# Kernel tuning notes

Hardware: AMD Instinct MI355X
Metric: run time of the kernel (lower is better)

## Reference

```python
import jax, jax.numpy as jnp
import numpy as np

B, K, C, H, W = 4, 100, 8, 128, 128
P = (C + 2) * C + C + C * C + C + C + 1  # 169 dynamic params per instance


def setup_inputs() -> dict:
    key = jax.random.key(0)
    k1, k2, k3 = jax.random.split(key, 3)
    seg_feat = jax.random.normal(k1, (B, C, H, W), dtype=jnp.float32)
    conv_weight = jax.random.normal(k2, (B, P, H, W), dtype=jnp.float32) * 0.1
    ind = jax.random.randint(k3, (B, K), 0, H * W)
    return {"seg_feat": seg_feat, "conv_weight": conv_weight, "ind": ind}


def _mask_head(seg_feat, conv_weight, ind):
    Bq, Cc, Hh, Ww = seg_feat.shape
    Kk = ind.shape[1]
    n = Bq * Kk
    HWl = Hh * Ww

    # _tranpose_and_gather_feat: [B,P,H,W] -> [B,HW,P] -> gather at ind -> [n,P]
    cw = conv_weight.reshape(Bq, -1, HWl).transpose(0, 2, 1)  # B,HW,P
    params = jnp.take_along_axis(cw, ind[:, :, None], axis=1).reshape(n, -1)

    # instance locations (x = ind % W, y = ind // W)
    xi = (ind % Ww).astype(jnp.float32)
    yi = (ind // Ww).astype(jnp.float32)
    loc = jnp.stack([xi, yi], axis=-1).reshape(n, 2)  # n,2

    # coords map, row-major (y outer, x inner), columns (x, y)
    y_grid, x_grid = jnp.meshgrid(jnp.arange(Hh, dtype=jnp.float32),
                                  jnp.arange(Ww, dtype=jnp.float32), indexing="ij")
    coords = jnp.stack([x_grid.reshape(-1), y_grid.reshape(-1)], axis=1)  # HW,2

    rel = (loc[:, None, :] - coords[None, :, :]).transpose(0, 2, 1) / 128.0  # n,2,HW

    # per-instance features: mask_feats[im_inds] -> [n, C, HW]
    feats = jnp.broadcast_to(seg_feat.reshape(Bq, 1, Cc, HWl), (Bq, Kk, Cc, HWl)).reshape(n, Cc, HWl)

    x = jnp.concatenate([rel, feats], axis=1)  # n, C+2, HW

    # parse dynamic params: weight_nums=[(C+2)*C, C*C, C], bias_nums=[C, C, 1]
    s0 = (Cc + 2) * Cc
    s1 = s0 + Cc * Cc
    s2 = s1 + Cc
    w0 = params[:, :s0].reshape(n, Cc, Cc + 2)
    w1 = params[:, s0:s1].reshape(n, Cc, Cc)
    w2 = params[:, s1:s2].reshape(n, 1, Cc)
    b0 = params[:, s2:s2 + Cc]
    b1 = params[:, s2 + Cc:s2 + 2 * Cc]
    b2 = params[:, s2 + 2 * Cc:]

    # grouped 1x1 convs == per-instance batched GEMMs
    h = jax.nn.relu(jnp.einsum("noc,ncL->noL", w0, x) + b0[:, :, None])
    h = jax.nn.relu(jnp.einsum("noc,ncL->noL", w1, h) + b1[:, :, None])
    logits = jnp.einsum("noc,ncL->noL", w2, h) + b2[:, :, None]  # n,1,HW
    return logits.reshape(Bq, Kk, Hh, Ww)


def reference(seg_feat, conv_weight, ind):
    logits = _mask_head(seg_feat, conv_weight, ind)
    return jax.nn.sigmoid(logits)  # B, K, H, W (is_train=False path)
```

## Files before the change

kernel.cpp:

```cpp
#include <hip/hip_runtime.h>
#include <hip/hip_fp16.h>
#include <math.h>

typedef unsigned int u32;
typedef __attribute__((ext_vector_type(8))) _Float16 f16x8;
typedef __attribute__((ext_vector_type(16))) float f32x16;

#define HW 16384
#define NB 4
#define NK 100
#define NGRP 25

__device__ __forceinline__ u32 pk2h(float lo, float hi) {
    return (u32)__half_as_ushort(__float2half_rn(lo))
         | ((u32)__half_as_ushort(__float2half_rn(hi)) << 16);
}
__device__ __forceinline__ void swap32(u32 &a, u32 &b) {
    asm("v_permlane32_swap_b32 %0, %1" : "+v"(a), "+v"(b));
}
__device__ __forceinline__ float rcpf(float x) {
    float r; asm("v_rcp_f32 %0, %1" : "=v"(r) : "v"(x)); return r;
}

__global__ __launch_bounds__(256) void pack_kernel(
    const float* __restrict__ cw, const int* __restrict__ ind,
    u32* __restrict__ A0, u32* __restrict__ A1, float* __restrict__ WT)
{
    int id = blockIdx.x * 256 + threadIdx.x;
    if (id < 25600) {
        int bg = id >> 8, rem = id & 255;
        int lane = rem >> 2, reg = rem & 3;
        int b = bg / NGRP, g = bg % NGRP;
        int row = lane & 31;
        int inst = g * 4 + (row >> 3);
        int ch = row & 7;
        int hw = ind[b * NK + inst];
        const float* base = cw + (size_t)b * 169 * HW + hw;
        float sx = (float)(hw & 127), sy = (float)(hw >> 7);
        float v[2];
        #pragma unroll
        for (int j = 0; j < 2; ++j) {
            int k = ((lane >> 5) << 3) + reg * 2 + j;
            float val = 0.f;
            if (k < 2)
                val = -base[(size_t)(ch * 10 + k) * HW] * 0.0078125f;
            else if (k < 10)
                val = base[(size_t)(ch * 10 + k) * HW];
            else if (k == 10)
                val = base[(size_t)(152 + ch) * HW]
                    + (base[(size_t)(ch * 10) * HW] * sx
                     + base[(size_t)(ch * 10 + 1) * HW] * sy) * 0.0078125f;
            v[j] = val;
        }
        A0[id] = pk2h(v[0], v[1]);
    } else if (id < 76800) {
        int id2 = id - 25600;
        int bg = id2 >> 9, r2 = id2 & 511;
        int frag = r2 >> 8;
        int lane = (r2 >> 2) & 63, reg = r2 & 3;
        int b = bg / NGRP, g = bg % NGRP;
        int row = lane & 31;
        int inst = g * 4 + (row >> 3);
        int hw = ind[b * NK + inst];
        const float* base = cw + (size_t)b * 169 * HW + hw;
        float v[2];
        #pragma unroll
        for (int j = 0; j < 2; ++j) {
            int k = ((lane >> 5) << 3) + reg * 2 + j;
            bool valid = ((row >> 4) == frag) && (((row >> 3) & 1) == (k >> 3));
            v[j] = valid ? base[(size_t)(80 + (row & 7) * 8 + (k & 7)) * HW] : 0.f;
        }
        A1[id2] = pk2h(v[0], v[1]);
    } else if (id < 84800) {
        int id3 = id - 76800;
        int bg = id3 / 80, q = id3 - bg * 80;
        int b = bg / NGRP, g = bg % NGRP;
        float val = 0.f;
        if (q < 32) {
            int hi = q >> 4, e = q & 15;
            int row = (e & 3) + 8 * (e >> 2) + 4 * hi;
            int inst = g * 4 + (row >> 3);
            int hw = ind[b * NK + inst];
            val = cw[(size_t)b * 169 * HW + (size_t)(160 + (row & 7)) * HW + hw];
        } else if (q < 64) {
            int half = (q - 32) >> 4, q2 = (q - 32) & 15;
            int n = q2 >> 2, j = q2 & 3;
            int hw = ind[b * NK + g * 4 + n];
            val = cw[(size_t)b * 169 * HW + (size_t)(144 + half * 4 + j) * HW + hw];
        } else if (q < 68) {
            int n = q - 64;
            int hw = ind[b * NK + g * 4 + n];
            val = 0.5f * cw[(size_t)b * 169 * HW + (size_t)168 * HW + hw];
        }
        WT[id3] = val;
    }
}

__global__ __launch_bounds__(64, 4) void mfma_kernel(
    const float* __restrict__ seg_feat,
    const u32* __restrict__ A0, const u32* __restrict__ A1,
    const float* __restrict__ WT, float* __restrict__ out)
{
    const int lane = threadIdx.x;
    const bool hi = lane >= 32;
    const int col = lane & 31;
    const int tile = blockIdx.x;
    const int b = blockIdx.y;
    const int g0 = blockIdx.z * 13;
    const int g1 = blockIdx.z ? NGRP : 13;

    const int px = tile * 32 + col;

    float f[8];
    #pragma unroll
    for (int c = 0; c < 8; ++c)
        f[c] = seg_feat[(size_t)(b * 8 + c) * HW + px];
    const float xp = (float)(px & 127), yp = (float)(px >> 7);

    u32 b0w0 = hi ? pk2h(f[6], f[7]) : pk2h(xp, yp);
    u32 b0w1 = hi ? 0x00003C00u : pk2h(f[0], f[1]);
    u32 b0w2 = hi ? 0u : pk2h(f[2], f[3]);
    u32 b0w3 = hi ? 0u : pk2h(f[4], f[5]);
    uint4 b0u = make_uint4(b0w0, b0w1, b0w2, b0w3);
    f16x8 B0 = __builtin_bit_cast(f16x8, b0u);

    f32x16 zero;
    #pragma unroll
    for (int i = 0; i < 16; ++i) zero[i] = 0.f;

    for (int g = g0; g < g1; ++g) {
        const int bg = b * NGRP + g;
        uint4 a0w  = ((const uint4*)A0)[bg * 64 + lane];
        uint4 a1aw = ((const uint4*)A1)[(bg * 2 + 0) * 64 + lane];
        uint4 a1bw = ((const uint4*)A1)[(bg * 2 + 1) * 64 + lane];
        const float* wb = WT + bg * 80;
        const float4* bi = (const float4*)(wb + (hi ? 16 : 0));
        float4 i0 = bi[0], i1 = bi[1], i2 = bi[2], i3 = bi[3];
        const float4* wv = (const float4*)(wb + 32 + (hi ? 16 : 0));
        float4 wn0 = wv[0], wn1 = wv[1], wn2 = wv[2], wn3 = wv[3];

        f32x16 d0 = __builtin_amdgcn_mfma_f32_32x32x16_f16(
            __builtin_bit_cast(f16x8, a0w), B0, zero, 0, 0, 0);

        u32 u0 = pk2h(fmaxf(d0[0], 0.f),  fmaxf(d0[1], 0.f));
        u32 u1 = pk2h(fmaxf(d0[2], 0.f),  fmaxf(d0[3], 0.f));
        u32 u2 = pk2h(fmaxf(d0[4], 0.f),  fmaxf(d0[5], 0.f));
        u32 u3 = pk2h(fmaxf(d0[6], 0.f),  fmaxf(d0[7], 0.f));
        u32 u4 = pk2h(fmaxf(d0[8], 0.f),  fmaxf(d0[9], 0.f));
        u32 u5 = pk2h(fmaxf(d0[10], 0.f), fmaxf(d0[11], 0.f));
        u32 u6 = pk2h(fmaxf(d0[12], 0.f), fmaxf(d0[13], 0.f));
        u32 u7 = pk2h(fmaxf(d0[14], 0.f), fmaxf(d0[15], 0.f));
        swap32(u0, u2);
        swap32(u1, u3);
        swap32(u4, u6);
        swap32(u5, u7);
        uint4 b1au = make_uint4(u0, u1, u2, u3);
        uint4 b1bu = make_uint4(u4, u5, u6, u7);

        f32x16 d1;
        d1[0] = i0.x; d1[1] = i0.y; d1[2]  = i0.z; d1[3]  = i0.w;
        d1[4] = i1.x; d1[5] = i1.y; d1[6]  = i1.z; d1[7]  = i1.w;
        d1[8] = i2.x; d1[9] = i2.y; d1[10] = i2.z; d1[11] = i2.w;
        d1[12] = i3.x; d1[13] = i3.y; d1[14] = i3.z; d1[15] = i3.w;
        d1 = __builtin_amdgcn_mfma_f32_32x32x16_f16(
            __builtin_bit_cast(f16x8, a1aw), __builtin_bit_cast(f16x8, b1au), d1, 0, 0, 0);
        d1 = __builtin_amdgcn_mfma_f32_32x32x16_f16(
            __builtin_bit_cast(f16x8, a1bw), __builtin_bit_cast(f16x8, b1bu), d1, 0, 0, 0);

        const float b2h0 = wb[64], b2h1 = wb[65], b2h2 = wb[66], b2h3 = wb[67];

        float pz0 = b2h0, pz1 = b2h1, pz2 = b2h2, pz3 = b2h3;
        pz0 = fmaf(wn0.x, fmaxf(d1[0], 0.f), pz0);
        pz0 = fmaf(wn0.y, fmaxf(d1[1], 0.f), pz0);
        pz0 = fmaf(wn0.z, fmaxf(d1[2], 0.f), pz0);
        pz0 = fmaf(wn0.w, fmaxf(d1[3], 0.f), pz0);
        pz1 = fmaf(wn1.x, fmaxf(d1[4], 0.f), pz1);
        pz1 = fmaf(wn1.y, fmaxf(d1[5], 0.f), pz1);
        pz1 = fmaf(wn1.z, fmaxf(d1[6], 0.f), pz1);
        pz1 = fmaf(wn1.w, fmaxf(d1[7], 0.f), pz1);
        pz2 = fmaf(wn2.x, fmaxf(d1[8], 0.f), pz2);
        pz2 = fmaf(wn2.y, fmaxf(d1[9], 0.f), pz2);
        pz2 = fmaf(wn2.z, fmaxf(d1[10], 0.f), pz2);
        pz2 = fmaf(wn2.w, fmaxf(d1[11], 0.f), pz2);
        pz3 = fmaf(wn3.x, fmaxf(d1[12], 0.f), pz3);
        pz3 = fmaf(wn3.y, fmaxf(d1[13], 0.f), pz3);
        pz3 = fmaf(wn3.z, fmaxf(d1[14], 0.f), pz3);
        pz3 = fmaf(wn3.w, fmaxf(d1[15], 0.f), pz3);

        u32 a01 = __builtin_bit_cast(u32, pz0), b01 = __builtin_bit_cast(u32, pz1);
        swap32(a01, b01);
        float z01 = __builtin_bit_cast(float, a01) + __builtin_bit_cast(float, b01);
        u32 a23 = __builtin_bit_cast(u32, pz2), b23 = __builtin_bit_cast(u32, pz3);
        swap32(a23, b23);
        float z23 = __builtin_bit_cast(float, a23) + __builtin_bit_cast(float, b23);

        float o01 = rcpf(1.f + __expf(-z01));
        float o23 = rcpf(1.f + __expf(-z23));

        size_t obase = (size_t)(b * NK + g * 4) * HW + px;
        out[obase + (size_t)(hi ? 1 : 0) * HW] = o01;
        out[obase + (size_t)(hi ? 3 : 2) * HW] = o23;
    }
}

extern "C" void kernel_launch(void* const* d_in, const int* in_sizes, int n_in,
                              void* d_out, int out_size, void* d_ws, size_t ws_size,
                              hipStream_t stream) {
    const float* seg_feat    = (const float*)d_in[0];
    const float* conv_weight = (const float*)d_in[1];
    const int*   ind         = (const int*)d_in[2];
    float*       out         = (float*)d_out;

    u32*   A0 = (u32*)d_ws;
    u32*   A1 = (u32*)((char*)d_ws + 102400);
    float* WT = (float*)((char*)d_ws + 307200);

    {
        dim3 grid((84800 + 255) / 256), block(256);
        pack_kernel<<<grid, block, 0, stream>>>(conv_weight, ind, A0, A1, WT);
    }
    {
        dim3 grid(512, 4, 2), block(64);
        mfma_kernel<<<grid, block, 0, stream>>>(seg_feat, A0, A1, WT, out);
    }
}
```

Measured before the change: 31.09 us.

## Process two pixel tiles per wave and split instance groups four ways

Each wave now handles 64 pixels, two 32-pixel MFMA tiles that share one load of the per-group packed weights and biases. This halves the weight-fetch traffic per pixel. The instance-group range is split across four z-blocks (7/6/6/6 groups) instead of two. v_permlane32_swap is replaced by __shfl_xor-based cross-half exchanges plus selects, which may cost more instructions or use LDS-backed permutes. The two independent MFMA chains per iteration also give the scheduler more instruction-level parallelism, at the price of more registers.

Result: faster. 28.52 us (-8.2%).

```diff
diff --git a/kernel.cpp b/kernel.cpp
--- a/kernel.cpp
+++ b/kernel.cpp
@@ -15,8 +15,11 @@
     return (u32)__half_as_ushort(__float2half_rn(lo))
          | ((u32)__half_as_ushort(__float2half_rn(hi)) << 16);
 }
-__device__ __forceinline__ void swap32(u32 &a, u32 &b) {
-    asm("v_permlane32_swap_b32 %0, %1" : "+v"(a), "+v"(b));
+__device__ __forceinline__ u32 sx32(u32 v) {
+    return (u32)__shfl_xor((int)v, 32, 64);
+}
+__device__ __forceinline__ float sx32f(float v) {
+    return __shfl_xor(v, 32, 64);
 }
 __device__ __forceinline__ float rcpf(float x) {
     float r; asm("v_rcp_f32 %0, %1" : "=v"(r) : "v"(x)); return r;
@@ -106,23 +109,32 @@
     const int col = lane & 31;
     const int tile = blockIdx.x;
     const int b = blockIdx.y;
-    const int g0 = blockIdx.z * 13;
-    const int g1 = blockIdx.z ? NGRP : 13;
-
-    const int px = tile * 32 + col;
-
-    float f[8];
+    const int z = blockIdx.z;
+    const int g0 = (z == 0) ? 0 : (6 * z + 1);
+    const int g1 = 6 * z + 7;
+
+    const int pxa = tile * 64 + col;
+    const int pxb = pxa + 32;
+
+    float fa[8], fb[8];
     #pragma unroll
-    for (int c = 0; c < 8; ++c)
-        f[c] = seg_feat[(size_t)(b * 8 + c) * HW + px];
-    const float xp = (float)(px & 127), yp = (float)(px >> 7);
-
-    u32 b0w0 = hi ? pk2h(f[6], f[7]) : pk2h(xp, yp);
-    u32 b0w1 = hi ? 0x00003C00u : pk2h(f[0], f[1]);
-    u32 b0w2 = hi ? 0u : pk2h(f[2], f[3]);
-    u32 b0w3 = hi ? 0u : pk2h(f[4], f[5]);
-    uint4 b0u = make_uint4(b0w0, b0w1, b0w2, b0w3);
-    f16x8 B0 = __builtin_bit_cast(f16x8, b0u);
+    for (int c = 0; c < 8; ++c) {
+        fa[c] = seg_feat[(size_t)(b * 8 + c) * HW + pxa];
+        fb[c] = seg_feat[(size_t)(b * 8 + c) * HW + pxb];
+    }
+    const float xpa = (float)(pxa & 127), ypa = (float)(pxa >> 7);
+    const float xpb = (float)(pxb & 127), ypb = (float)(pxb >> 7);
+
+    uint4 b0ua = make_uint4(hi ? pk2h(fa[6], fa[7]) : pk2h(xpa, ypa),
+                            hi ? 0x00003C00u : pk2h(fa[0], fa[1]),
+                            hi ? 0u : pk2h(fa[2], fa[3]),
+                            hi ? 0u : pk2h(fa[4], fa[5]));
+    uint4 b0ub = make_uint4(hi ? pk2h(fb[6], fb[7]) : pk2h(xpb, ypb),
+                            hi ? 0x00003C00u : pk2h(fb[0], fb[1]),
+                            hi ? 0u : pk2h(fb[2], fb[3]),
+                            hi ? 0u : pk2h(fb[4], fb[5]));
+    f16x8 B0a = __builtin_bit_cast(f16x8, b0ua);
+    f16x8 B0b = __builtin_bit_cast(f16x8, b0ub);
 
     f32x16 zero;
     #pragma unroll
@@ -138,68 +150,130 @@
         float4 i0 = bi[0], i1 = bi[1], i2 = bi[2], i3 = bi[3];
         const float4* wv = (const float4*)(wb + 32 + (hi ? 16 : 0));
         float4 wn0 = wv[0], wn1 = wv[1], wn2 = wv[2], wn3 = wv[3];
-
-        f32x16 d0 = __builtin_amdgcn_mfma_f32_32x32x16_f16(
-            __builtin_bit_cast(f16x8, a0w), B0, zero, 0, 0, 0);
-
-        u32 u0 = pk2h(fmaxf(d0[0], 0.f),  fmaxf(d0[1], 0.f));
-        u32 u1 = pk2h(fmaxf(d0[2], 0.f),  fmaxf(d0[3], 0.f));
-        u32 u2 = pk2h(fmaxf(d0[4], 0.f),  fmaxf(d0[5], 0.f));
-        u32 u3 = pk2h(fmaxf(d0[6], 0.f),  fmaxf(d0[7], 0.f));
-        u32 u4 = pk2h(fmaxf(d0[8], 0.f),  fmaxf(d0[9], 0.f));
-        u32 u5 = pk2h(fmaxf(d0[10], 0.f), fmaxf(d0[11], 0.f));
-        u32 u6 = pk2h(fmaxf(d0[12], 0.f), fmaxf(d0[13], 0.f));
-        u32 u7 = pk2h(fmaxf(d0[14], 0.f), fmaxf(d0[15], 0.f));
-        swap32(u0, u2);
-        swap32(u1, u3);
-        swap32(u4, u6);
-        swap32(u5, u7);
-        uint4 b1au = make_uint4(u0, u1, u2, u3);
-        uint4 b1bu = make_uint4(u4, u5, u6, u7);
-
-        f32x16 d1;
-        d1[0] = i0.x; d1[1] = i0.y; d1[2]  = i0.z; d1[3]  = i0.w;
-        d1[4] = i1.x; d1[5] = i1.y; d1[6]  = i1.z; d1[7]  = i1.w;
-        d1[8] = i2.x; d1[9] = i2.y; d1[10] = i2.z; d1[11] = i2.w;
-        d1[12] = i3.x; d1[13] = i3.y; d1[14] = i3.z; d1[15] = i3.w;
-        d1 = __builtin_amdgcn_mfma_f32_32x32x16_f16(
-            __builtin_bit_cast(f16x8, a1aw), __builtin_bit_cast(f16x8, b1au), d1, 0, 0, 0);
-        d1 = __builtin_amdgcn_mfma_f32_32x32x16_f16(
-            __builtin_bit_cast(f16x8, a1bw), __builtin_bit_cast(f16x8, b1bu), d1, 0, 0, 0);
-
-        const float b2h0 = wb[64], b2h1 = wb[65], b2h2 = wb[66], b2h3 = wb[67];
-
-        float pz0 = b2h0, pz1 = b2h1, pz2 = b2h2, pz3 = b2h3;
-        pz0 = fmaf(wn0.x, fmaxf(d1[0], 0.f), pz0);
-        pz0 = fmaf(wn0.y, fmaxf(d1[1], 0.f), pz0);
-        pz0 = fmaf(wn0.z, fmaxf(d1[2], 0.f), pz0);
-        pz0 = fmaf(wn0.w, fmaxf(d1[3], 0.f), pz0);
-        pz1 = fmaf(wn1.x, fmaxf(d1[4], 0.f), pz1);
-        pz1 = fmaf(wn1.y, fmaxf(d1[5], 0.f), pz1);
-        pz1 = fmaf(wn1.z, fmaxf(d1[6], 0.f), pz1);
-        pz1 = fmaf(wn1.w, fmaxf(d1[7], 0.f), pz1);
-        pz2 = fmaf(wn2.x, fmaxf(d1[8], 0.f), pz2);
-        pz2 = fmaf(wn2.y, fmaxf(d1[9], 0.f), pz2);
-        pz2 = fmaf(wn2.z, fmaxf(d1[10], 0.f), pz2);
-        pz2 = fmaf(wn2.w, fmaxf(d1[11], 0.f), pz2);
-        pz3 = fmaf(wn3.x, fmaxf(d1[12], 0.f), pz3);
-        pz3 = fmaf(wn3.y, fmaxf(d1[13], 0.f), pz3);
-        pz3 = fmaf(wn3.z, fmaxf(d1[14], 0.f), pz3);
-        pz3 = fmaf(wn3.w, fmaxf(d1[15], 0.f), pz3);
-
-        u32 a01 = __builtin_bit_cast(u32, pz0), b01 = __builtin_bit_cast(u32, pz1);
-        swap32(a01, b01);
-        float z01 = __builtin_bit_cast(float, a01) + __builtin_bit_cast(float, b01);
-        u32 a23 = __builtin_bit_cast(u32, pz2), b23 = __builtin_bit_cast(u32, pz3);
-        swap32(a23, b23);
-        float z23 = __builtin_bit_cast(float, a23) + __builtin_bit_cast(float, b23);
-
-        float o01 = rcpf(1.f + __expf(-z01));
-        float o23 = rcpf(1.f + __expf(-z23));
-
-        size_t obase = (size_t)(b * NK + g * 4) * HW + px;
-        out[obase + (size_t)(hi ? 1 : 0) * HW] = o01;
-        out[obase + (size_t)(hi ? 3 : 2) * HW] = o23;
+        float4 bw = *(const float4*)(wb + 64);
+
+        {
+            f32x16 d0 = __builtin_amdgcn_mfma_f32_32x32x16_f16(
+                __builtin_bit_cast(f16x8, a0w), B0a, zero, 0, 0, 0);
+
+            u32 u0 = pk2h(fmaxf(d0[0], 0.f),  fmaxf(d0[1], 0.f));
+            u32 u1 = pk2h(fmaxf(d0[2], 0.f),  fmaxf(d0[3], 0.f));
+            u32 u2 = pk2h(fmaxf(d0[4], 0.f),  fmaxf(d0[5], 0.f));
+            u32 u3 = pk2h(fmaxf(d0[6], 0.f),  fmaxf(d0[7], 0.f));
+            u32 u4 = pk2h(fmaxf(d0[8], 0.f),  fmaxf(d0[9], 0.f));
+            u32 u5 = pk2h(fmaxf(d0[10], 0.f), fmaxf(d0[11], 0.f));
+            u32 u6 = pk2h(fmaxf(d0[12], 0.f), fmaxf(d0[13], 0.f));
+            u32 u7 = pk2h(fmaxf(d0[14], 0.f), fmaxf(d0[15], 0.f));
+            u32 t0 = sx32(u0), t1 = sx32(u1), t2 = sx32(u2), t3 = sx32(u3);
+            u32 t4 = sx32(u4), t5 = sx32(u5), t6 = sx32(u6), t7 = sx32(u7);
+            uint4 b1au = make_uint4(hi ? t2 : u0, hi ? t3 : u1,
+                                    hi ? u2 : t0, hi ? u3 : t1);
+            uint4 b1bu = make_uint4(hi ? t6 : u4, hi ? t7 : u5,
+                                    hi ? u6 : t4, hi ? u7 : t5);
+
+            f32x16 d1;
+            d1[0]  = i0.x; d1[1]  = i0.y; d1[2]  = i0.z; d1[3]  = i0.w;
+            d1[4]  = i1.x; d1[5]  = i1.y; d1[6]  = i1.z; d1[7]  = i1.w;
+            d1[8]  = i2.x; d1[9]  = i2.y; d1[10] = i2.z; d1[11] = i2.w;
+            d1[12] = i3.x; d1[13] = i3.y; d1[14] = i3.z; d1[15] = i3.w;
+            d1 = __builtin_amdgcn_mfma_f32_32x32x16_f16(
+                __builtin_bit_cast(f16x8, a1aw), __builtin_bit_cast(f16x8, b1au), d1, 0, 0, 0);
+            d1 = __builtin_amdgcn_mfma_f32_32x32x16_f16(
+                __builtin_bit_cast(f16x8, a1bw), __builtin_bit_cast(f16x8, b1bu), d1, 0, 0, 0);
+
+            float pz0 = bw.x, pz1 = bw.y, pz2 = bw.z, pz3 = bw.w;
+            pz0 = fmaf(wn0.x, fmaxf(d1[0], 0.f), pz0);
+            pz0 = fmaf(wn0.y, fmaxf(d1[1], 0.f), pz0);
+            pz0 = fmaf(wn0.z, fmaxf(d1[2], 0.f), pz0);
+            pz0 = fmaf(wn0.w, fmaxf(d1[3], 0.f), pz0);
+            pz1 = fmaf(wn1.x, fmaxf(d1[4], 0.f), pz1);
+            pz1 = fmaf(wn1.y, fmaxf(d1[5], 0.f), pz1);
+            pz1 = fmaf(wn1.z, fmaxf(d1[6], 0.f), pz1);
+            pz1 = fmaf(wn1.w, fmaxf(d1[7], 0.f), pz1);
+            pz2 = fmaf(wn2.x, fmaxf(d1[8], 0.f), pz2);
+            pz2 = fmaf(wn2.y, fmaxf(d1[9], 0.f), pz2);
+            pz2 = fmaf(wn2.z, fmaxf(d1[10], 0.f), pz2);
+            pz2 = fmaf(wn2.w, fmaxf(d1[11], 0.f), pz2);
+            pz3 = fmaf(wn3.x, fmaxf(d1[12], 0.f), pz3);
+            pz3 = fmaf(wn3.y, fmaxf(d1[13], 0.f), pz3);
+            pz3 = fmaf(wn3.z, fmaxf(d1[14], 0.f), pz3);
+            pz3 = fmaf(wn3.w, fmaxf(d1[15], 0.f), pz3);
+
+            float zi0 = pz0 + sx32f(pz0);
+            float zi1 = pz1 + sx32f(pz1);
+            float zi2 = pz2 + sx32f(pz2);
+            float zi3 = pz3 + sx32f(pz3);
+            float z01 = hi ? zi1 : zi0;
+            float z23 = hi ? zi3 : zi2;
+
+            float o01 = rcpf(1.f + __expf(-z01));
+            float o23 = rcpf(1.f + __expf(-z23));
+
+            size_t obase = (size_t)(b * NK + g * 4) * HW + pxa;
+            out[obase + (size_t)(hi ? 1 : 0) * HW] = o01;
+            out[obase + (size_t)(hi ? 3 : 2) * HW] = o23;
+        }
+        {
+            f32x16 d0 = __builtin_amdgcn_mfma_f32_32x32x16_f16(
+                __builtin_bit_cast(f16x8, a0w), B0b, zero, 0, 0, 0);
+
+            u32 u0 = pk2h(fmaxf(d0[0], 0.f),  fmaxf(d0[1], 0.f));
+            u32 u1 = pk2h(fmaxf(d0[2], 0.f),  fmaxf(d0[3], 0.f));
+            u32 u2 = pk2h(fmaxf(d0[4], 0.f),  fmaxf(d0[5], 0.f));
+            u32 u3 = pk2h(fmaxf(d0[6], 0.f),  fmaxf(d0[7], 0.f));
+            u32 u4 = pk2h(fmaxf(d0[8], 0.f),  fmaxf(d0[9], 0.f));
+            u32 u5 = pk2h(fmaxf(d0[10], 0.f), fmaxf(d0[11], 0.f));
+            u32 u6 = pk2h(fmaxf(d0[12], 0.f), fmaxf(d0[13], 0.f));
+            u32 u7 = pk2h(fmaxf(d0[14], 0.f), fmaxf(d0[15], 0.f));
+            u32 t0 = sx32(u0), t1 = sx32(u1), t2 = sx32(u2), t3 = sx32(u3);
+            u32 t4 = sx32(u4), t5 = sx32(u5), t6 = sx32(u6), t7 = sx32(u7);
+            uint4 b1au = make_uint4(hi ? t2 : u0, hi ? t3 : u1,
+                                    hi ? u2 : t0, hi ? u3 : t1);
+            uint4 b1bu = make_uint4(hi ? t6 : u4, hi ? t7 : u5,
+                                    hi ? u6 : t4, hi ? u7 : t5);
+
+            f32x16 d1;
+            d1[0]  = i0.x; d1[1]  = i0.y; d1[2]  = i0.z; d1[3]  = i0.w;
+            d1[4]  = i1.x; d1[5]  = i1.y; d1[6]  = i1.z; d1[7]  = i1.w;
+            d1[8]  = i2.x; d1[9]  = i2.y; d1[10] = i2.z; d1[11] = i2.w;
+            d1[12] = i3.x; d1[13] = i3.y; d1[14] = i3.z; d1[15] = i3.w;
+            d1 = __builtin_amdgcn_mfma_f32_32x32x16_f16(
+                __builtin_bit_cast(f16x8, a1aw), __builtin_bit_cast(f16x8, b1au), d1, 0, 0, 0);
+            d1 = __builtin_amdgcn_mfma_f32_32x32x16_f16(
+                __builtin_bit_cast(f16x8, a1bw), __builtin_bit_cast(f16x8, b1bu), d1, 0, 0, 0);
+
+            float pz0 = bw.x, pz1 = bw.y, pz2 = bw.z, pz3 = bw.w;
+            pz0 = fmaf(wn0.x, fmaxf(d1[0], 0.f), pz0);
+            pz0 = fmaf(wn0.y, fmaxf(d1[1], 0.f), pz0);
+            pz0 = fmaf(wn0.z, fmaxf(d1[2], 0.f), pz0);
+            pz0 = fmaf(wn0.w, fmaxf(d1[3], 0.f), pz0);
+            pz1 = fmaf(wn1.x, fmaxf(d1[4], 0.f), pz1);
+            pz1 = fmaf(wn1.y, fmaxf(d1[5], 0.f), pz1);
+            pz1 = fmaf(wn1.z, fmaxf(d1[6], 0.f), pz1);
+            pz1 = fmaf(wn1.w, fmaxf(d1[7], 0.f), pz1);
+            pz2 = fmaf(wn2.x, fmaxf(d1[8], 0.f), pz2);
+            pz2 = fmaf(wn2.y, fmaxf(d1[9], 0.f), pz2);
+            pz2 = fmaf(wn2.z, fmaxf(d1[10], 0.f), pz2);
+            pz2 = fmaf(wn2.w, fmaxf(d1[11], 0.f), pz2);
+            pz3 = fmaf(wn3.x, fmaxf(d1[12], 0.f), pz3);
+            pz3 = fmaf(wn3.y, fmaxf(d1[13], 0.f), pz3);
+            pz3 = fmaf(wn3.z, fmaxf(d1[14], 0.f), pz3);
+            pz3 = fmaf(wn3.w, fmaxf(d1[15], 0.f), pz3);
+
+            float zi0 = pz0 + sx32f(pz0);
+            float zi1 = pz1 + sx32f(pz1);
+            float zi2 = pz2 + sx32f(pz2);
+            float zi3 = pz3 + sx32f(pz3);
+            float z01 = hi ? zi1 : zi0;
+            float z23 = hi ? zi3 : zi2;
+
+            float o01 = rcpf(1.f + __expf(-z01));
+            float o23 = rcpf(1.f + __expf(-z23));
+
+            size_t obase = (size_t)(b * NK + g * 4) * HW + pxb;
+            out[obase + (size_t)(hi ? 1 : 0) * HW] = o01;
+            out[obase + (size_t)(hi ? 3 : 2) * HW] = o23;
+        }
     }
 }
 
@@ -220,7 +294,7 @@
         pack_kernel<<<grid, block, 0, stream>>>(conv_weight, ind, A0, A1, WT);
     }
     {
-        dim3 grid(512, 4, 2), block(64);
+        dim3 grid(256, 4, 4), block(64);
         mfma_kernel<<<grid, block, 0, stream>>>(seg_feat, A0, A1, WT, out);
     }
 }
```

## Process four pixel tiles per wave to reuse per-group weights; use shfl_xor swaps

Applied to the files above, without the earlier changes.

Each wave now handles 128 pixels (four 32-pixel sub-tiles) and loads each group's A0/A1/WT parameters once for all four, cutting redundant parameter loads. The grid changes from 512x4x2 to 128x4x4, so each block covers 6-7 groups instead of 12-13. The permlane32 swap is replaced by __shfl_xor with select, which may lower to slower ds_bpermute or DPP ops. Register pressure goes up with four B0 operands held live.

New measurement: 29.93 us. -3.7%, faster.

```diff
diff --git a/kernel.cpp b/kernel.cpp
--- a/kernel.cpp
+++ b/kernel.cpp
@@ -15,8 +15,11 @@
     return (u32)__half_as_ushort(__float2half_rn(lo))
          | ((u32)__half_as_ushort(__float2half_rn(hi)) << 16);
 }
-__device__ __forceinline__ void swap32(u32 &a, u32 &b) {
-    asm("v_permlane32_swap_b32 %0, %1" : "+v"(a), "+v"(b));
+__device__ __forceinline__ u32 sx32(u32 v) {
+    return (u32)__shfl_xor((int)v, 32, 64);
+}
+__device__ __forceinline__ float sx32f(float v) {
+    return __shfl_xor(v, 32, 64);
 }
 __device__ __forceinline__ float rcpf(float x) {
     float r; asm("v_rcp_f32 %0, %1" : "=v"(r) : "v"(x)); return r;
@@ -106,23 +109,27 @@
     const int col = lane & 31;
     const int tile = blockIdx.x;
     const int b = blockIdx.y;
-    const int g0 = blockIdx.z * 13;
-    const int g1 = blockIdx.z ? NGRP : 13;
-
-    const int px = tile * 32 + col;
-
-    float f[8];
+    const int z = blockIdx.z;
+    const int g0 = (z == 0) ? 0 : (6 * z + 1);
+    const int g1 = 6 * z + 7;
+
+    const int px0 = tile * 128 + col;
+
+    f16x8 B0[4];
     #pragma unroll
-    for (int c = 0; c < 8; ++c)
-        f[c] = seg_feat[(size_t)(b * 8 + c) * HW + px];
-    const float xp = (float)(px & 127), yp = (float)(px >> 7);
-
-    u32 b0w0 = hi ? pk2h(f[6], f[7]) : pk2h(xp, yp);
-    u32 b0w1 = hi ? 0x00003C00u : pk2h(f[0], f[1]);
-    u32 b0w2 = hi ? 0u : pk2h(f[2], f[3]);
-    u32 b0w3 = hi ? 0u : pk2h(f[4], f[5]);
-    uint4 b0u = make_uint4(b0w0, b0w1, b0w2, b0w3);
-    f16x8 B0 = __builtin_bit_cast(f16x8, b0u);
+    for (int t = 0; t < 4; ++t) {
+        const int px = px0 + 32 * t;
+        float f[8];
+        #pragma unroll
+        for (int c = 0; c < 8; ++c)
+            f[c] = seg_feat[(size_t)(b * 8 + c) * HW + px];
+        const float xp = (float)(px & 127), yp = (float)(px >> 7);
+        uint4 b0u = make_uint4(hi ? pk2h(f[6], f[7]) : pk2h(xp, yp),
+                               hi ? 0x00003C00u : pk2h(f[0], f[1]),
+                               hi ? 0u : pk2h(f[2], f[3]),
+                               hi ? 0u : pk2h(f[4], f[5]));
+        B0[t] = __builtin_bit_cast(f16x8, b0u);
+    }
 
     f32x16 zero;
     #pragma unroll
@@ -138,68 +145,72 @@
         float4 i0 = bi[0], i1 = bi[1], i2 = bi[2], i3 = bi[3];
         const float4* wv = (const float4*)(wb + 32 + (hi ? 16 : 0));
         float4 wn0 = wv[0], wn1 = wv[1], wn2 = wv[2], wn3 = wv[3];
-
-        f32x16 d0 = __builtin_amdgcn_mfma_f32_32x32x16_f16(
-            __builtin_bit_cast(f16x8, a0w), B0, zero, 0, 0, 0);
-
-        u32 u0 = pk2h(fmaxf(d0[0], 0.f),  fmaxf(d0[1], 0.f));
-        u32 u1 = pk2h(fmaxf(d0[2], 0.f),  fmaxf(d0[3], 0.f));
-        u32 u2 = pk2h(fmaxf(d0[4], 0.f),  fmaxf(d0[5], 0.f));
-        u32 u3 = pk2h(fmaxf(d0[6], 0.f),  fmaxf(d0[7], 0.f));
-        u32 u4 = pk2h(fmaxf(d0[8], 0.f),  fmaxf(d0[9], 0.f));
-        u32 u5 = pk2h(fmaxf(d0[10], 0.f), fmaxf(d0[11], 0.f));
-        u32 u6 = pk2h(fmaxf(d0[12], 0.f), fmaxf(d0[13], 0.f));
-        u32 u7 = pk2h(fmaxf(d0[14], 0.f), fmaxf(d0[15], 0.f));
-        swap32(u0, u2);
-        swap32(u1, u3);
-        swap32(u4, u6);
-        swap32(u5, u7);
-        uint4 b1au = make_uint4(u0, u1, u2, u3);
-        uint4 b1bu = make_uint4(u4, u5, u6, u7);
-
-        f32x16 d1;
-        d1[0] = i0.x; d1[1] = i0.y; d1[2]  = i0.z; d1[3]  = i0.w;
-        d1[4] = i1.x; d1[5] = i1.y; d1[6]  = i1.z; d1[7]  = i1.w;
-        d1[8] = i2.x; d1[9] = i2.y; d1[10] = i2.z; d1[11] = i2.w;
-        d1[12] = i3.x; d1[13] = i3.y; d1[14] = i3.z; d1[15] = i3.w;
-        d1 = __builtin_amdgcn_mfma_f32_32x32x16_f16(
-            __builtin_bit_cast(f16x8, a1aw), __builtin_bit_cast(f16x8, b1au), d1, 0, 0, 0);
-        d1 = __builtin_amdgcn_mfma_f32_32x32x16_f16(
-            __builtin_bit_cast(f16x8, a1bw), __builtin_bit_cast(f16x8, b1bu), d1, 0, 0, 0);
-
-        const float b2h0 = wb[64], b2h1 = wb[65], b2h2 = wb[66], b2h3 = wb[67];
-
-        float pz0 = b2h0, pz1 = b2h1, pz2 = b2h2, pz3 = b2h3;
-        pz0 = fmaf(wn0.x, fmaxf(d1[0], 0.f), pz0);
-        pz0 = fmaf(wn0.y, fmaxf(d1[1], 0.f), pz0);
-        pz0 = fmaf(wn0.z, fmaxf(d1[2], 0.f), pz0);
-        pz0 = fmaf(wn0.w, fmaxf(d1[3], 0.f), pz0);
-        pz1 = fmaf(wn1.x, fmaxf(d1[4], 0.f), pz1);
-        pz1 = fmaf(wn1.y, fmaxf(d1[5], 0.f), pz1);
-        pz1 = fmaf(wn1.z, fmaxf(d1[6], 0.f), pz1);
-        pz1 = fmaf(wn1.w, fmaxf(d1[7], 0.f), pz1);
-        pz2 = fmaf(wn2.x, fmaxf(d1[8], 0.f), pz2);
-        pz2 = fmaf(wn2.y, fmaxf(d1[9], 0.f), pz2);
-        pz2 = fmaf(wn2.z, fmaxf(d1[10], 0.f), pz2);
-        pz2 = fmaf(wn2.w, fmaxf(d1[11], 0.f), pz2);
-        pz3 = fmaf(wn3.x, fmaxf(d1[12], 0.f), pz3);
-        pz3 = fmaf(wn3.y, fmaxf(d1[13], 0.f), pz3);
-        pz3 = fmaf(wn3.z, fmaxf(d1[14], 0.f), pz3);
-        pz3 = fmaf(wn3.w, fmaxf(d1[15], 0.f), pz3);
-
-        u32 a01 = __builtin_bit_cast(u32, pz0), b01 = __builtin_bit_cast(u32, pz1);
-        swap32(a01, b01);
-        float z01 = __builtin_bit_cast(float, a01) + __builtin_bit_cast(float, b01);
-        u32 a23 = __builtin_bit_cast(u32, pz2), b23 = __builtin_bit_cast(u32, pz3);
-        swap32(a23, b23);
-        float z23 = __builtin_bit_cast(float, a23) + __builtin_bit_cast(float, b23);
-
-        float o01 = rcpf(1.f + __expf(-z01));
-        float o23 = rcpf(1.f + __expf(-z23));
-
-        size_t obase = (size_t)(b * NK + g * 4) * HW + px;
-        out[obase + (size_t)(hi ? 1 : 0) * HW] = o01;
-        out[obase + (size_t)(hi ? 3 : 2) * HW] = o23;
+        float4 bw = *(const float4*)(wb + 64);
+
+        #pragma unroll
+        for (int t = 0; t < 4; ++t) {
+            const int px = px0 + 32 * t;
+
+            f32x16 d0 = __builtin_amdgcn_mfma_f32_32x32x16_f16(
+                __builtin_bit_cast(f16x8, a0w), B0[t], zero, 0, 0, 0);
+
+            u32 u0 = pk2h(fmaxf(d0[0], 0.f),  fmaxf(d0[1], 0.f));
+            u32 u1 = pk2h(fmaxf(d0[2], 0.f),  fmaxf(d0[3], 0.f));
+            u32 u2 = pk2h(fmaxf(d0[4], 0.f),  fmaxf(d0[5], 0.f));
+            u32 u3 = pk2h(fmaxf(d0[6], 0.f),  fmaxf(d0[7], 0.f));
+            u32 u4 = pk2h(fmaxf(d0[8], 0.f),  fmaxf(d0[9], 0.f));
+            u32 u5 = pk2h(fmaxf(d0[10], 0.f), fmaxf(d0[11], 0.f));
+            u32 u6 = pk2h(fmaxf(d0[12], 0.f), fmaxf(d0[13], 0.f));
+            u32 u7 = pk2h(fmaxf(d0[14], 0.f), fmaxf(d0[15], 0.f));
+            u32 t0 = sx32(u0), t1 = sx32(u1), t2 = sx32(u2), t3 = sx32(u3);
+            u32 t4 = sx32(u4), t5 = sx32(u5), t6 = sx32(u6), t7 = sx32(u7);
+            uint4 b1au = make_uint4(hi ? t2 : u0, hi ? t3 : u1,
+                                    hi ? u2 : t0, hi ? u3 : t1);
+            uint4 b1bu = make_uint4(hi ? t6 : u4, hi ? t7 : u5,
+                                    hi ? u6 : t4, hi ? u7 : t5);
+
+            f32x16 d1;
+            d1[0]  = i0.x; d1[1]  = i0.y; d1[2]  = i0.z; d1[3]  = i0.w;
+            d1[4]  = i1.x; d1[5]  = i1.y; d1[6]  = i1.z; d1[7]  = i1.w;
+            d1[8]  = i2.x; d1[9]  = i2.y; d1[10] = i2.z; d1[11] = i2.w;
+            d1[12] = i3.x; d1[13] = i3.y; d1[14] = i3.z; d1[15] = i3.w;
+            d1 = __builtin_amdgcn_mfma_f32_32x32x16_f16(
+                __builtin_bit_cast(f16x8, a1aw), __builtin_bit_cast(f16x8, b1au), d1, 0, 0, 0);
+            d1 = __builtin_amdgcn_mfma_f32_32x32x16_f16(
+                __builtin_bit_cast(f16x8, a1bw), __builtin_bit_cast(f16x8, b1bu), d1, 0, 0, 0);
+
+            float pz0 = bw.x, pz1 = bw.y, pz2 = bw.z, pz3 = bw.w;
+            pz0 = fmaf(wn0.x, fmaxf(d1[0], 0.f), pz0);
+            pz0 = fmaf(wn0.y, fmaxf(d1[1], 0.f), pz0);
+            pz0 = fmaf(wn0.z, fmaxf(d1[2], 0.f), pz0);
+            pz0 = fmaf(wn0.w, fmaxf(d1[3], 0.f), pz0);
+            pz1 = fmaf(wn1.x, fmaxf(d1[4], 0.f), pz1);
+            pz1 = fmaf(wn1.y, fmaxf(d1[5], 0.f), pz1);
+            pz1 = fmaf(wn1.z, fmaxf(d1[6], 0.f), pz1);
+            pz1 = fmaf(wn1.w, fmaxf(d1[7], 0.f), pz1);
+            pz2 = fmaf(wn2.x, fmaxf(d1[8], 0.f), pz2);
+            pz2 = fmaf(wn2.y, fmaxf(d1[9], 0.f), pz2);
+            pz2 = fmaf(wn2.z, fmaxf(d1[10], 0.f), pz2);
+            pz2 = fmaf(wn2.w, fmaxf(d1[11], 0.f), pz2);
+            pz3 = fmaf(wn3.x, fmaxf(d1[12], 0.f), pz3);
+            pz3 = fmaf(wn3.y, fmaxf(d1[13], 0.f), pz3);
+            pz3 = fmaf(wn3.z, fmaxf(d1[14], 0.f), pz3);
+            pz3 = fmaf(wn3.w, fmaxf(d1[15], 0.f), pz3);
+
+            float zi0 = pz0 + sx32f(pz0);
+            float zi1 = pz1 + sx32f(pz1);
+            float zi2 = pz2 + sx32f(pz2);
+            float zi3 = pz3 + sx32f(pz3);
+            float z01 = hi ? zi1 : zi0;
+            float z23 = hi ? zi3 : zi2;
+
+            float o01 = rcpf(1.f + __expf(-z01));
+            float o23 = rcpf(1.f + __expf(-z23));
+
+            size_t obase = (size_t)(b * NK + g * 4) * HW + px;
+            out[obase + (size_t)(hi ? 1 : 0) * HW] = o01;
+            out[obase + (size_t)(hi ? 3 : 2) * HW] = o23;
+        }
     }
 }
 
@@ -220,7 +231,7 @@
         pack_kernel<<<grid, block, 0, stream>>>(conv_weight, ind, A0, A1, WT);
     }
     {
-        dim3 grid(512, 4, 2), block(64);
+        dim3 grid(128, 4, 4), block(64);
         mfma_kernel<<<grid, block, 0, stream>>>(seg_feat, A0, A1, WT, out);
     }
 }
```
